# Optimization experiments

Hardware: AMD Instinct MI355X
Metric: run time of the kernel (lower is better)

The kernel has to match this reference:

```python
import jax, jax.numpy as jnp
import numpy as np

H = 300  # hidden size hardcoded in the module
VX = 32000
VY = 32000
NX, NY, B = 128, 128, 256


def setup_inputs() -> dict:
    key = jax.random.key(0)
    ks = jax.random.split(key, 10)
    s = 1.0 / np.sqrt(H)
    x = jax.random.randint(ks[0], (NX, B), 0, VX)
    y = jax.random.randint(ks[1], (NY, B), 0, VY)
    # padding_idx=0: zero the pad row of each embedding table
    enc_emb = jax.random.normal(ks[2], (VX, H), jnp.float32).at[0].set(0.0)
    encW = jax.random.uniform(ks[3], (H, H), jnp.float32, -s, s)
    encb = jax.random.uniform(ks[4], (H,), jnp.float32, -s, s)
    dec_emb = jax.random.normal(ks[5], (VY, H), jnp.float32).at[0].set(0.0)
    decW = jax.random.uniform(ks[6], (H, H), jnp.float32, -s, s)
    decb = jax.random.uniform(ks[7], (H,), jnp.float32, -s, s)
    outW = jax.random.uniform(ks[8], (VY, H), jnp.float32, -s, s)
    outb = jax.random.uniform(ks[9], (VY,), jnp.float32, -s, s)
    return {"x": x, "y": y, "enc_emb": enc_emb, "encW": encW, "encb": encb,
            "dec_emb": dec_emb, "decW": decW, "decb": decb,
            "outW": outW, "outb": outb}


def reference(x, y, enc_emb, encW, encb, dec_emb, decW, decb, outW, outb):
    # Encoder: Elman recurrence h = relu(e_x[i] + W h + b)
    e_x = enc_emb[x]                                  # [NX, B, H]
    h0 = jnp.zeros((x.shape[1], H), e_x.dtype)        # h=0 broadcast over batch

    def enc_step(h, ex):
        return jax.nn.relu(ex + h @ encW.T + encb), None

    h, _ = jax.lax.scan(enc_step, h0, e_x)

    # Decoder: teacher-forced recurrence with per-step mean cross-entropy
    e_y = dec_emb[y]                                  # [NY, B, H]

    def dec_step(h, inp):
        ey, tgt = inp
        h = jax.nn.relu(ey + h @ decW.T + decb)
        logits = h @ outW.T + outb                    # [B, VY]
        logp = jax.nn.log_softmax(logits, axis=-1)
        ce = -jnp.mean(jnp.take_along_axis(logp, tgt[:, None], axis=-1))
        return h, ce

    _, ces = jax.lax.scan(dec_step, h, (e_y[:-1], y[1:]))
    return jnp.sum(ces)
```

## Files before the change

### kernel.cpp

```cpp
#include <hip/hip_runtime.h>
#include <hip/hip_bf16.h>
#include <stdint.h>

typedef unsigned short u16;
typedef unsigned char u8;
typedef float f32x4 __attribute__((ext_vector_type(4)));
typedef float f32x2 __attribute__((ext_vector_type(2)));
typedef _Float16 f16x2 __attribute__((ext_vector_type(2)));
typedef _Float16 f16x8 __attribute__((ext_vector_type(8)));

#define H      300
#define KP     320
#define BATCH  256
#define NX     128
#define NY     128
#define VY     32000
#define NPAD   32768
#define MROWS  32512


#define OWS_OFF   0UL
#define OWS_BYTES ((unsigned long)NPAD * KP)
#define OWS_PAD   131072UL
#define A8_OFF    (OWS_OFF + OWS_BYTES + OWS_PAD)
#define A8_BYTES  ((unsigned long)MROWS * KP)
#define WTE_OFF   (A8_OFF + A8_BYTES)
#define WT_BYTES  (320UL * KP * 4)
#define WTD_OFF   (WTE_OFF + WT_BYTES)
#define OBP_OFF   (WTD_OFF + WT_BYTES)
#define OBP_BYTES ((unsigned long)NPAD * 4)
#define SE_OFF    (OBP_OFF + OBP_BYTES)
#define SE_BYTES  ((unsigned long)MROWS * 4)

#define ASYNC_COPY16(dst_lds, src_glb)                                          \
    __builtin_amdgcn_global_load_lds(                                           \
        (const __attribute__((address_space(1))) unsigned int*)(src_glb),       \
        (__attribute__((address_space(3))) unsigned int*)(dst_lds), 16, 0, 0)

__global__ __launch_bounds__(256) void k0_prep(const float* __restrict__ outW,
                                               const float* __restrict__ encW,
                                               const float* __restrict__ decW,
                                               const float* __restrict__ outb,
                                               u8* __restrict__ ows,
                                               float* __restrict__ eob,
                                               float* __restrict__ wte,
                                               float* __restrict__ wtd) {
    long id = (long)blockIdx.x * 256 + threadIdx.x;
    const long n1 = (long)NPAD * KP / 4;
    if (id < n1) {
        int v = (int)(id / 80), k4 = (int)(id % 80) * 4;
        float4 f = {0.f, 0.f, 0.f, 0.f};
        if (v < VY && k4 < H) f = *(const float4*)&outW[(long)v * H + k4];
        int w = __builtin_amdgcn_cvt_pk_fp8_f32(f.x, f.y, 0, false);
        w = __builtin_amdgcn_cvt_pk_fp8_f32(f.z, f.w, w, true);
        long dst = (long)(v >> 6) * 20480 + (k4 >> 5) * 2048 + ((v >> 4) & 3) * 512
                 + (v & 15) * 8 + ((k4 >> 3) & 3) * 128 + (k4 & 7);
        *(unsigned int*)(ows + dst) = (unsigned int)w;
        return;
    }
    long id2 = id - n1;
    if (id2 < NPAD) {
        eob[id2] = (id2 < VY) ? __expf(outb[id2]) : 0.f;
        return;
    }
    id2 -= NPAD;
    if (id2 < 320L * KP) {
        int k = (int)(id2 / KP), j = (int)(id2 % KP);
        wte[id2] = (k < H && j < H) ? encW[j * H + k] : 0.f;
        return;
    }
    id2 -= 320L * KP;
    if (id2 < 320L * KP) {
        int k = (int)(id2 / KP), j = (int)(id2 % KP);
        wtd[id2] = (k < H && j < H) ? decW[j * H + k] : 0.f;
    }
}

__global__ __launch_bounds__(640) void k1_rnn(const int* __restrict__ x,
                                              const int* __restrict__ y,
                                              const float* __restrict__ enc_emb,
                                              const float* __restrict__ dec_emb,
                                              const float* __restrict__ encb,
                                              const float* __restrict__ decb,
                                              const float* __restrict__ wte,
                                              const float* __restrict__ wtd,
                                              u8* __restrict__ A8) {
    const int tid = threadIdx.x;
    const int s = tid / 160;
    const int j = tid - s * 160;
    const int b = blockIdx.x;

    __shared__ __align__(16) _Float16 hh[320];
    __shared__ float part[1280];
    __shared__ __align__(4) u8 a8row[320];

    for (int i = tid; i < 320; i += 640) hh[i] = (_Float16)0.f;

    const bool comb = (tid < 320);
    const int jc = tid;
    const float be = (comb && jc < H) ? encb[jc] : 0.f;
    const float bd = (comb && jc < H) ? decb[jc] : 0.f;

    f16x2 wa[40], wc[40];
#pragma unroll
    for (int kk = 0; kk < 40; ++kk) {
        int k0 = s * 80 + 2 * kk;
        wa[kk] = (f16x2){(_Float16)wte[k0 * KP + j],       (_Float16)wte[(k0 + 1) * KP + j]};
        wc[kk] = (f16x2){(_Float16)wte[k0 * KP + j + 160], (_Float16)wte[(k0 + 1) * KP + j + 160]};
    }

    int idx_n = x[BATCH + b];
    float e_cur = 0.f;
    if (comb && jc < H) e_cur = enc_emb[(long)x[b] * H + jc];
    __syncthreads();

    const f16x8* hb8 = (const f16x8*)&hh[s * 80];

    for (int t = 0; t < NX; ++t) {
        int idx_n2 = x[min(t + 2, NX - 1) * BATCH + b];
        float e_nx = 0.f;
        if (comb && jc < H && t + 1 < NX) e_nx = enc_emb[(long)idx_n * H + jc];

        float p0 = 0.f, p1 = 0.f;
#pragma unroll
        for (int i = 0; i < 10; ++i) {
            f16x8 hv = hb8[i];
            f16x2 q0 = {hv[0], hv[1]}, q1 = {hv[2], hv[3]};
            f16x2 q2 = {hv[4], hv[5]}, q3 = {hv[6], hv[7]};
            p0 = __builtin_amdgcn_fdot2(wa[4 * i + 0], q0, p0, false);
            p1 = __builtin_amdgcn_fdot2(wc[4 * i + 0], q0, p1, false);
            p0 = __builtin_amdgcn_fdot2(wa[4 * i + 1], q1, p0, false);
            p1 = __builtin_amdgcn_fdot2(wc[4 * i + 1], q1, p1, false);
            p0 = __builtin_amdgcn_fdot2(wa[4 * i + 2], q2, p0, false);
            p1 = __builtin_amdgcn_fdot2(wc[4 * i + 2], q2, p1, false);
            p0 = __builtin_amdgcn_fdot2(wa[4 * i + 3], q3, p0, false);
            p1 = __builtin_amdgcn_fdot2(wc[4 * i + 3], q3, p1, false);
        }
        part[s * 320 + j] = p0;
        part[s * 320 + 160 + j] = p1;
        __syncthreads();
        if (comb) {
            float v = part[jc] + part[320 + jc] + part[640 + jc] + part[960 + jc] + be + e_cur;
            hh[jc] = (_Float16)fmaxf(v, 0.f);
        }
        __syncthreads();
        e_cur = e_nx; idx_n = idx_n2;
    }

#pragma unroll
    for (int kk = 0; kk < 40; ++kk) {
        int k0 = s * 80 + 2 * kk;
        wa[kk] = (f16x2){(_Float16)wtd[k0 * KP + j],       (_Float16)wtd[(k0 + 1) * KP + j]};
        wc[kk] = (f16x2){(_Float16)wtd[k0 * KP + j + 160], (_Float16)wtd[(k0 + 1) * KP + j + 160]};
    }

    idx_n = y[BATCH + b];
    e_cur = 0.f;
    if (comb && jc < H) e_cur = dec_emb[(long)y[b] * H + jc];

    for (int t = 0; t < NY - 1; ++t) {
        int idx_n2 = y[min(t + 2, NY - 1) * BATCH + b];
        float e_nx = 0.f;
        if (comb && jc < H && t + 1 < NY - 1) e_nx = dec_emb[(long)idx_n * H + jc];

        float p0 = 0.f, p1 = 0.f;
#pragma unroll
        for (int i = 0; i < 10; ++i) {
            f16x8 hv = hb8[i];
            f16x2 q0 = {hv[0], hv[1]}, q1 = {hv[2], hv[3]};
            f16x2 q2 = {hv[4], hv[5]}, q3 = {hv[6], hv[7]};
            p0 = __builtin_amdgcn_fdot2(wa[4 * i + 0], q0, p0, false);
            p1 = __builtin_amdgcn_fdot2(wc[4 * i + 0], q0, p1, false);
            p0 = __builtin_amdgcn_fdot2(wa[4 * i + 1], q1, p0, false);
            p1 = __builtin_amdgcn_fdot2(wc[4 * i + 1], q1, p1, false);
            p0 = __builtin_amdgcn_fdot2(wa[4 * i + 2], q2, p0, false);
            p1 = __builtin_amdgcn_fdot2(wc[4 * i + 2], q2, p1, false);
            p0 = __builtin_amdgcn_fdot2(wa[4 * i + 3], q3, p0, false);
            p1 = __builtin_amdgcn_fdot2(wc[4 * i + 3], q3, p1, false);
        }
        part[s * 320 + j] = p0;
        part[s * 320 + 160 + j] = p1;
        __syncthreads();
        if (comb) {
            float v = part[jc] + part[320 + jc] + part[640 + jc] + part[960 + jc] + bd + e_cur;
            v = fmaxf(v, 0.f);
            hh[jc] = (_Float16)v;
            int pk = __builtin_amdgcn_cvt_pk_fp8_f32(v, v, 0, false);
            a8row[jc] = (u8)(pk & 0xff);
        }
        __syncthreads();
        if (tid < 80)
            ((unsigned int*)(A8 + (long)(t * BATCH + b) * KP))[tid] =
                ((const unsigned int*)a8row)[tid];
        e_cur = e_nx; idx_n = idx_n2;
    }
}

__global__ __launch_bounds__(256, 2) void k2_gemm(const u8* __restrict__ A8,
                                                  const u8* __restrict__ OWS,
                                                  const float* __restrict__ eob,
                                                  float* __restrict__ sumexp) {
    const int tid = threadIdx.x;
    const int lane = tid & 63, wave = tid >> 6;
    const int lane16 = lane & 15, quad = lane >> 4;
    const int bid = blockIdx.x;
    const int cg8 = bid & 7;
    const int cs  = (bid >> 3) & 3;
    const int rb  = bid >> 5;
    const int colbase = cg8 * 4096 + cs * 1024;
    const long tile0 = (long)(colbase >> 6);

    __shared__ __align__(16) u8 bt[2][20480];

    long a[4][10];
    {
        const u8* abase = A8 + ((long)rb * 256 + wave * 64 + lane16) * KP + quad * 8;
#pragma unroll
        for (int rt = 0; rt < 4; ++rt)
#pragma unroll
            for (int ks = 0; ks < 10; ++ks)
                a[rt][ks] = *(const long*)(abase + rt * 16 * KP + ks * 32);
    }

    {
        const u8* src = OWS + tile0 * 20480 + (wave << 10) + (lane << 4);
        u8* dst = &bt[0][wave << 10];
#pragma unroll
        for (int r = 0; r < 5; ++r)
            ASYNC_COPY16(dst + r * 4096, src + r * 4096);
    }

    float rsum[16];
#pragma unroll
    for (int i = 0; i < 16; ++i) rsum[i] = 0.f;

    f32x4 accLo[4][2], accHi[4][2];

#pragma unroll 1
    for (int ct = 0; ct < 16; ++ct) {
        __syncthreads();
        if (ct < 15) {
            const u8* src = OWS + (tile0 + ct + 1) * 20480 + (wave << 10) + (lane << 4);
            u8* dst = &bt[(ct + 1) & 1][wave << 10];
#pragma unroll
            for (int r = 0; r < 5; ++r)
                ASYNC_COPY16(dst + r * 4096, src + r * 4096);
        }
        const u8* bb = &bt[ct & 1][0];

#pragma unroll
        for (int p = 0; p < 4; ++p)
#pragma unroll
            for (int q = 0; q < 2; ++q) accLo[p][q] = (f32x4){0.f, 0.f, 0.f, 0.f};
#pragma unroll
        for (int ks = 0; ks < 10; ++ks) {
            long b0 = *(const long*)(bb + ks * 2048 + 0 * 512 + lane * 8);
            long b1 = *(const long*)(bb + ks * 2048 + 1 * 512 + lane * 8);
#pragma unroll
            for (int rt = 0; rt < 4; ++rt) {
                accLo[rt][0] = __builtin_amdgcn_mfma_f32_16x16x32_fp8_fp8(
                    a[rt][ks], b0, accLo[rt][0], 0, 0, 0);
                accLo[rt][1] = __builtin_amdgcn_mfma_f32_16x16x32_fp8_fp8(
                    a[rt][ks], b1, accLo[rt][1], 0, 0, 0);
            }
        }
        if (ct > 0) {
            int cbp = colbase + (ct - 1) * 64;
#pragma unroll
            for (int tc = 0; tc < 2; ++tc) {
                float eb = eob[cbp + (tc + 2) * 16 + lane16];
#pragma unroll
                for (int rt = 0; rt < 4; ++rt)
#pragma unroll
                    for (int i = 0; i < 4; ++i)
                        rsum[rt * 4 + i] += __expf(accHi[rt][tc][i]) * eb;
            }
        }

#pragma unroll
        for (int p = 0; p < 4; ++p)
#pragma unroll
            for (int q = 0; q < 2; ++q) accHi[p][q] = (f32x4){0.f, 0.f, 0.f, 0.f};
#pragma unroll
        for (int ks = 0; ks < 10; ++ks) {
            long b2 = *(const long*)(bb + ks * 2048 + 2 * 512 + lane * 8);
            long b3 = *(const long*)(bb + ks * 2048 + 3 * 512 + lane * 8);
#pragma unroll
            for (int rt = 0; rt < 4; ++rt) {
                accHi[rt][0] = __builtin_amdgcn_mfma_f32_16x16x32_fp8_fp8(
                    a[rt][ks], b2, accHi[rt][0], 0, 0, 0);
                accHi[rt][1] = __builtin_amdgcn_mfma_f32_16x16x32_fp8_fp8(
                    a[rt][ks], b3, accHi[rt][1], 0, 0, 0);
            }
        }
        {
            int cb = colbase + ct * 64;
#pragma unroll
            for (int tc = 0; tc < 2; ++tc) {
                float eb = eob[cb + tc * 16 + lane16];
#pragma unroll
                for (int rt = 0; rt < 4; ++rt)
#pragma unroll
                    for (int i = 0; i < 4; ++i)
                        rsum[rt * 4 + i] += __expf(accLo[rt][tc][i]) * eb;
            }
        }
    }

    {
        int cb = colbase + 15 * 64;
#pragma unroll
        for (int tc = 0; tc < 2; ++tc) {
            float eb = eob[cb + (tc + 2) * 16 + lane16];
#pragma unroll
            for (int rt = 0; rt < 4; ++rt)
#pragma unroll
                for (int i = 0; i < 4; ++i)
                    rsum[rt * 4 + i] += __expf(accHi[rt][tc][i]) * eb;
        }
    }

#pragma unroll
    for (int m = 1; m < 16; m <<= 1)
#pragma unroll
        for (int i = 0; i < 16; ++i) rsum[i] += __shfl_xor(rsum[i], m, 64);
    if (lane16 == 0) {
        float* sp = &sumexp[(long)rb * 256 + wave * 64];
#pragma unroll
        for (int rt = 0; rt < 4; ++rt)
#pragma unroll
            for (int i = 0; i < 4; ++i)
                atomicAdd(&sp[rt * 16 + quad * 4 + i], rsum[rt * 4 + i]);
    }
}

__global__ __launch_bounds__(256) void k3_ce(const u8* __restrict__ A8,
                                             const u8* __restrict__ OWS,
                                             const float* __restrict__ outb,
                                             const float* __restrict__ sumexp,
                                             const int* __restrict__ y,
                                             float* __restrict__ out) {
    const int wave = threadIdx.x >> 6, lane = threadIdx.x & 63;
    const int r = blockIdx.x * 4 + wave;
    const int t = r >> 8, b = r & 255;
    const int tgt = y[(t + 1) * BATCH + b];
    float s = 0.f;
    if (lane < 40) {
        unsigned long long av = *(const unsigned long long*)(A8 + (long)r * KP + lane * 8);
        long wdst = (long)(tgt >> 6) * 20480 + (lane >> 2) * 2048
                  + ((tgt >> 4) & 3) * 512 + (tgt & 15) * 8 + (lane & 3) * 128;
        unsigned long long wv = *(const unsigned long long*)(OWS + wdst);
        unsigned int a4 = (unsigned int)av, a4h = (unsigned int)(av >> 32);
        unsigned int w4 = (unsigned int)wv, w4h = (unsigned int)(wv >> 32);
        f32x2 al = __builtin_amdgcn_cvt_pk_f32_fp8(a4, false);
        f32x2 ah = __builtin_amdgcn_cvt_pk_f32_fp8(a4, true);
        f32x2 wl = __builtin_amdgcn_cvt_pk_f32_fp8(w4, false);
        f32x2 wh = __builtin_amdgcn_cvt_pk_f32_fp8(w4, true);
        s += al[0] * wl[0] + al[1] * wl[1] + ah[0] * wh[0] + ah[1] * wh[1];
        al = __builtin_amdgcn_cvt_pk_f32_fp8(a4h, false);
        ah = __builtin_amdgcn_cvt_pk_f32_fp8(a4h, true);
        wl = __builtin_amdgcn_cvt_pk_f32_fp8(w4h, false);
        wh = __builtin_amdgcn_cvt_pk_f32_fp8(w4h, true);
        s += al[0] * wl[0] + al[1] * wl[1] + ah[0] * wh[0] + ah[1] * wh[1];
    }
#pragma unroll
    for (int m = 1; m < 64; m <<= 1) s += __shfl_xor(s, m, 64);
    __shared__ float part[4];
    if (lane == 0) part[wave] = logf(sumexp[r]) - (s + outb[tgt]);
    __syncthreads();
    if (threadIdx.x == 0) {
        float tot = part[0] + part[1] + part[2] + part[3];
        atomicAdd(out, tot * (1.0f / 256.0f));
    }
}

extern "C" void kernel_launch(void* const* d_in, const int* in_sizes, int n_in,
                              void* d_out, int out_size, void* d_ws, size_t ws_size,
                              hipStream_t stream) {
    (void)in_sizes; (void)n_in; (void)out_size; (void)ws_size;
    const int*   x       = (const int*)d_in[0];
    const int*   y       = (const int*)d_in[1];
    const float* enc_emb = (const float*)d_in[2];
    const float* encW    = (const float*)d_in[3];
    const float* encb    = (const float*)d_in[4];
    const float* dec_emb = (const float*)d_in[5];
    const float* decW    = (const float*)d_in[6];
    const float* decb    = (const float*)d_in[7];
    const float* outW    = (const float*)d_in[8];
    const float* outb    = (const float*)d_in[9];

    char* ws = (char*)d_ws;
    u8* ows  = (u8*)(ws + OWS_OFF);
    u8* A8   = (u8*)(ws + A8_OFF);
    float* wte    = (float*)(ws + WTE_OFF);
    float* wtd    = (float*)(ws + WTD_OFF);
    float* eob    = (float*)(ws + OBP_OFF);
    float* sumexp = (float*)(ws + SE_OFF);

    hipMemsetAsync(sumexp, 0, SE_BYTES, stream);
    hipMemsetAsync(d_out, 0, sizeof(float), stream);

    long n0 = (long)NPAD * KP / 4 + NPAD + 2L * 320 * KP;
    k0_prep<<<(int)((n0 + 255) / 256), 256, 0, stream>>>(outW, encW, decW, outb,
                                                         ows, eob, wte, wtd);
    k1_rnn<<<256, 640, 0, stream>>>(x, y, enc_emb, dec_emb, encb, decb, wte, wtd, A8);
    k2_gemm<<<127 * 32, 256, 0, stream>>>(A8, ows, eob, sumexp);
    k3_ce<<<8128, 256, 0, stream>>>(A8, ows, outb, sumexp, y, (float*)d_out);
}
```

Before: 960.0 us.

## Batch 16 sequences per block and compute RNN recurrence with MFMA

The recurrent kernel changes from one batch element per block, which used fdot2 partial sums and a cross-thread reduction with two barriers per step, to 16 batch rows per block. Each step's hidden-state update becomes a 16x16x32 f16 MFMA, with weights held in registers and a double-buffered hidden state in shared memory, so each step needs one barrier. The grid drops from 256 to 16 blocks, leaving most CUs idle during the serial recurrence. The aim is to shorten the latency of each serial step at the cost of parallelism. Embedding gathers are no longer prefetched a step ahead, and FP8 writes to A8 become per-byte stores.

```diff
diff --git a/kernel.cpp b/kernel.cpp
--- a/kernel.cpp
+++ b/kernel.cpp
@@ -86,113 +86,116 @@
                                               const float* __restrict__ wtd,
                                               u8* __restrict__ A8) {
     const int tid = threadIdx.x;
-    const int s = tid / 160;
-    const int j = tid - s * 160;
-    const int b = blockIdx.x;
-
-    __shared__ __align__(16) _Float16 hh[320];
-    __shared__ float part[1280];
-    __shared__ __align__(4) u8 a8row[320];
-
-    for (int i = tid; i < 320; i += 640) hh[i] = (_Float16)0.f;
-
-    const bool comb = (tid < 320);
-    const int jc = tid;
-    const float be = (comb && jc < H) ? encb[jc] : 0.f;
-    const float bd = (comb && jc < H) ? decb[jc] : 0.f;
-
-    f16x2 wa[40], wc[40];
-#pragma unroll
-    for (int kk = 0; kk < 40; ++kk) {
-        int k0 = s * 80 + 2 * kk;
-        wa[kk] = (f16x2){(_Float16)wte[k0 * KP + j],       (_Float16)wte[(k0 + 1) * KP + j]};
-        wc[kk] = (f16x2){(_Float16)wte[k0 * KP + j + 160], (_Float16)wte[(k0 + 1) * KP + j + 160]};
-    }
-
-    int idx_n = x[BATCH + b];
-    float e_cur = 0.f;
-    if (comb && jc < H) e_cur = enc_emb[(long)x[b] * H + jc];
+    const int wave = tid >> 6, lane = tid & 63;
+    const int lane16 = lane & 15, quad = lane >> 4;
+    const int b0 = blockIdx.x * 16;
+    const int col0 = wave * 32;
+    const int c0 = col0 + lane16, c1 = col0 + 16 + lane16;
+
+    __shared__ __align__(16) _Float16 hbuf[2][16][328];
+
+    for (int i = tid; i < 2 * 16 * 328; i += 640)
+        ((_Float16*)hbuf)[i] = (_Float16)0.f;
+
+    const float be0 = (c0 < H) ? encb[c0] : 0.f;
+    const float be1 = (c1 < H) ? encb[c1] : 0.f;
+
+    f16x8 bw[10][2];
+#pragma unroll
+    for (int kt = 0; kt < 10; ++kt)
+#pragma unroll
+        for (int tc = 0; tc < 2; ++tc) {
+            const int cc = col0 + tc * 16 + lane16;
+            f16x8 v;
+#pragma unroll
+            for (int jj = 0; jj < 8; ++jj)
+                v[jj] = (_Float16)wte[(kt * 32 + quad * 8 + jj) * KP + cc];
+            bw[kt][tc] = v;
+        }
+
     __syncthreads();
 
-    const f16x8* hb8 = (const f16x8*)&hh[s * 80];
+    int idxv[4];
+#pragma unroll
+    for (int i = 0; i < 4; ++i) idxv[i] = x[b0 + quad * 4 + i];
 
     for (int t = 0; t < NX; ++t) {
-        int idx_n2 = x[min(t + 2, NX - 1) * BATCH + b];
-        float e_nx = 0.f;
-        if (comb && jc < H && t + 1 < NX) e_nx = enc_emb[(long)idx_n * H + jc];
-
-        float p0 = 0.f, p1 = 0.f;
-#pragma unroll
-        for (int i = 0; i < 10; ++i) {
-            f16x8 hv = hb8[i];
-            f16x2 q0 = {hv[0], hv[1]}, q1 = {hv[2], hv[3]};
-            f16x2 q2 = {hv[4], hv[5]}, q3 = {hv[6], hv[7]};
-            p0 = __builtin_amdgcn_fdot2(wa[4 * i + 0], q0, p0, false);
-            p1 = __builtin_amdgcn_fdot2(wc[4 * i + 0], q0, p1, false);
-            p0 = __builtin_amdgcn_fdot2(wa[4 * i + 1], q1, p0, false);
-            p1 = __builtin_amdgcn_fdot2(wc[4 * i + 1], q1, p1, false);
-            p0 = __builtin_amdgcn_fdot2(wa[4 * i + 2], q2, p0, false);
-            p1 = __builtin_amdgcn_fdot2(wc[4 * i + 2], q2, p1, false);
-            p0 = __builtin_amdgcn_fdot2(wa[4 * i + 3], q3, p0, false);
-            p1 = __builtin_amdgcn_fdot2(wc[4 * i + 3], q3, p1, false);
-        }
-        part[s * 320 + j] = p0;
-        part[s * 320 + 160 + j] = p1;
+        float e0[4], e1[4];
+#pragma unroll
+        for (int i = 0; i < 4; ++i) {
+            e0[i] = (c0 < H) ? enc_emb[(long)idxv[i] * H + c0] : 0.f;
+            e1[i] = (c1 < H) ? enc_emb[(long)idxv[i] * H + c1] : 0.f;
+        }
+        int tn = min(t + 1, NX - 1);
+#pragma unroll
+        for (int i = 0; i < 4; ++i) idxv[i] = x[tn * BATCH + b0 + quad * 4 + i];
+
+        const _Float16* hb = &hbuf[t & 1][0][0];
+        f32x4 acc0 = {0.f, 0.f, 0.f, 0.f}, acc1 = {0.f, 0.f, 0.f, 0.f};
+#pragma unroll
+        for (int kt = 0; kt < 10; ++kt) {
+            f16x8 af = *(const f16x8*)(hb + lane16 * 328 + kt * 32 + quad * 8);
+            acc0 = __builtin_amdgcn_mfma_f32_16x16x32_f16(af, bw[kt][0], acc0, 0, 0, 0);
+            acc1 = __builtin_amdgcn_mfma_f32_16x16x32_f16(af, bw[kt][1], acc1, 0, 0, 0);
+        }
+        _Float16* hn = &hbuf[(t + 1) & 1][0][0];
+#pragma unroll
+        for (int i = 0; i < 4; ++i) {
+            int row = quad * 4 + i;
+            hn[row * 328 + c0] = (_Float16)fmaxf(acc0[i] + be0 + e0[i], 0.f);
+            hn[row * 328 + c1] = (_Float16)fmaxf(acc1[i] + be1 + e1[i], 0.f);
+        }
         __syncthreads();
-        if (comb) {
-            float v = part[jc] + part[320 + jc] + part[640 + jc] + part[960 + jc] + be + e_cur;
-            hh[jc] = (_Float16)fmaxf(v, 0.f);
+    }
+
+#pragma unroll
+    for (int kt = 0; kt < 10; ++kt)
+#pragma unroll
+        for (int tc = 0; tc < 2; ++tc) {
+            const int cc = col0 + tc * 16 + lane16;
+            f16x8 v;
+#pragma unroll
+            for (int jj = 0; jj < 8; ++jj)
+                v[jj] = (_Float16)wtd[(kt * 32 + quad * 8 + jj) * KP + cc];
+            bw[kt][tc] = v;
+        }
+    const float bd0 = (c0 < H) ? decb[c0] : 0.f;
+    const float bd1 = (c1 < H) ? decb[c1] : 0.f;
+#pragma unroll
+    for (int i = 0; i < 4; ++i) idxv[i] = y[b0 + quad * 4 + i];
+
+    for (int t = 0; t < NY - 1; ++t) {
+        float e0[4], e1[4];
+#pragma unroll
+        for (int i = 0; i < 4; ++i) {
+            e0[i] = (c0 < H) ? dec_emb[(long)idxv[i] * H + c0] : 0.f;
+            e1[i] = (c1 < H) ? dec_emb[(long)idxv[i] * H + c1] : 0.f;
+        }
+        int tn = min(t + 1, NY - 2);
+#pragma unroll
+        for (int i = 0; i < 4; ++i) idxv[i] = y[tn * BATCH + b0 + quad * 4 + i];
+
+        const _Float16* hb = &hbuf[t & 1][0][0];
+        f32x4 acc0 = {0.f, 0.f, 0.f, 0.f}, acc1 = {0.f, 0.f, 0.f, 0.f};
+#pragma unroll
+        for (int kt = 0; kt < 10; ++kt) {
+            f16x8 af = *(const f16x8*)(hb + lane16 * 328 + kt * 32 + quad * 8);
+            acc0 = __builtin_amdgcn_mfma_f32_16x16x32_f16(af, bw[kt][0], acc0, 0, 0, 0);
+            acc1 = __builtin_amdgcn_mfma_f32_16x16x32_f16(af, bw[kt][1], acc1, 0, 0, 0);
+        }
+        _Float16* hn = &hbuf[(t + 1) & 1][0][0];
+#pragma unroll
+        for (int i = 0; i < 4; ++i) {
+            int row = quad * 4 + i;
+            float v0 = fmaxf(acc0[i] + bd0 + e0[i], 0.f);
+            float v1 = fmaxf(acc1[i] + bd1 + e1[i], 0.f);
+            hn[row * 328 + c0] = (_Float16)v0;
+            hn[row * 328 + c1] = (_Float16)v1;
+            long rbase = (long)(t * BATCH + b0 + row) * KP;
+            A8[rbase + c0] = (u8)(__builtin_amdgcn_cvt_pk_fp8_f32(v0, v0, 0, false) & 0xff);
+            A8[rbase + c1] = (u8)(__builtin_amdgcn_cvt_pk_fp8_f32(v1, v1, 0, false) & 0xff);
         }
         __syncthreads();
-        e_cur = e_nx; idx_n = idx_n2;
-    }
-
-#pragma unroll
-    for (int kk = 0; kk < 40; ++kk) {
-        int k0 = s * 80 + 2 * kk;
-        wa[kk] = (f16x2){(_Float16)wtd[k0 * KP + j],       (_Float16)wtd[(k0 + 1) * KP + j]};
-        wc[kk] = (f16x2){(_Float16)wtd[k0 * KP + j + 160], (_Float16)wtd[(k0 + 1) * KP + j + 160]};
-    }
-
-    idx_n = y[BATCH + b];
-    e_cur = 0.f;
-    if (comb && jc < H) e_cur = dec_emb[(long)y[b] * H + jc];
-
-    for (int t = 0; t < NY - 1; ++t) {
-        int idx_n2 = y[min(t + 2, NY - 1) * BATCH + b];
-        float e_nx = 0.f;
-        if (comb && jc < H && t + 1 < NY - 1) e_nx = dec_emb[(long)idx_n * H + jc];
-
-        float p0 = 0.f, p1 = 0.f;
-#pragma unroll
-        for (int i = 0; i < 10; ++i) {
-            f16x8 hv = hb8[i];
-            f16x2 q0 = {hv[0], hv[1]}, q1 = {hv[2], hv[3]};
-            f16x2 q2 = {hv[4], hv[5]}, q3 = {hv[6], hv[7]};
-            p0 = __builtin_amdgcn_fdot2(wa[4 * i + 0], q0, p0, false);
-            p1 = __builtin_amdgcn_fdot2(wc[4 * i + 0], q0, p1, false);
-            p0 = __builtin_amdgcn_fdot2(wa[4 * i + 1], q1, p0, false);
-            p1 = __builtin_amdgcn_fdot2(wc[4 * i + 1], q1, p1, false);
-            p0 = __builtin_amdgcn_fdot2(wa[4 * i + 2], q2, p0, false);
-            p1 = __builtin_amdgcn_fdot2(wc[4 * i + 2], q2, p1, false);
-            p0 = __builtin_amdgcn_fdot2(wa[4 * i + 3], q3, p0, false);
-            p1 = __builtin_amdgcn_fdot2(wc[4 * i + 3], q3, p1, false);
-        }
-        part[s * 320 + j] = p0;
-        part[s * 320 + 160 + j] = p1;
-        __syncthreads();
-        if (comb) {
-            float v = part[jc] + part[320 + jc] + part[640 + jc] + part[960 + jc] + bd + e_cur;
-            v = fmaxf(v, 0.f);
-            hh[jc] = (_Float16)v;
-            int pk = __builtin_amdgcn_cvt_pk_fp8_f32(v, v, 0, false);
-            a8row[jc] = (u8)(pk & 0xff);
-        }
-        __syncthreads();
-        if (tid < 80)
-            ((unsigned int*)(A8 + (long)(t * BATCH + b) * KP))[tid] =
-                ((const unsigned int*)a8row)[tid];
-        e_cur = e_nx; idx_n = idx_n2;
     }
 }
 
@@ -403,7 +406,7 @@
     long n0 = (long)NPAD * KP / 4 + NPAD + 2L * 320 * KP;
     k0_prep<<<(int)((n0 + 255) / 256), 256, 0, stream>>>(outW, encW, decW, outb,
                                                          ows, eob, wte, wtd);
-    k1_rnn<<<256, 640, 0, stream>>>(x, y, enc_emb, dec_emb, encb, decb, wte, wtd, A8);
+    k1_rnn<<<16, 640, 0, stream>>>(x, y, enc_emb, dec_emb, encb, decb, wte, wtd, A8);
     k2_gemm<<<127 * 32, 256, 0, stream>>>(A8, ows, eob, sumexp);
     k3_ce<<<8128, 256, 0, stream>>>(A8, ows, outb, sumexp, y, (float*)d_out);
 }
```

Measured after the change: 1.299 ms. 35.3% more time.
